# Kernel optimization log

Hardware: AMD Instinct MI355X
Metric: run time of the kernel (lower is better)

The kernel has to match this reference:

```python
import jax, jax.numpy as jnp
import numpy as np

N_NODES = 50000
N_EDGES = 800000
NFEAT, NHID1, NHID2, NHID3, NCLASS = 128, 128, 128, 64, 32


def _glorot(key, fan_in, fan_out):
    lim = 1.0 / np.sqrt(fan_in)
    return jax.random.uniform(key, (fan_in, fan_out), jnp.float32, -lim, lim)


def setup_inputs() -> dict:
    key = jax.random.key(0)
    ks = jax.random.split(key, 12)
    x = jax.random.normal(ks[0], (N_NODES, NFEAT), jnp.float32)
    edge_src = jax.random.randint(ks[1], (N_EDGES,), 0, N_NODES, jnp.int32)
    edge_dst = jax.random.randint(ks[2], (N_EDGES,), 0, N_NODES, jnp.int32)
    edge_val = jax.random.uniform(ks[3], (N_EDGES,), jnp.float32)
    W1 = _glorot(ks[4], NFEAT, NHID1)
    W2 = _glorot(ks[5], NHID1, NHID2)
    W3 = _glorot(ks[6], NHID2, NHID3)
    W4 = _glorot(ks[7], NHID3, NCLASS)
    b1 = jnp.zeros((NHID1,), jnp.float32)
    b2 = jnp.zeros((NHID2,), jnp.float32)
    b3 = jnp.zeros((NHID3,), jnp.float32)
    b4 = jnp.zeros((NCLASS,), jnp.float32)
    return {"x": x, "edge_src": edge_src, "edge_dst": edge_dst, "edge_val": edge_val,
            "W1": W1, "b1": b1, "W2": W2, "b2": b2, "W3": W3, "b3": b3, "W4": W4, "b4": b4}


def _gc_layer(h, W, b, src, dst, val):
    # support = h @ W ; out = adj @ support + b  (adj in COO form)
    support = h @ W                                   # [N, d_out]
    msgs = support[src] * val[:, None]                # [E, d_out] irregular gather
    agg = jax.ops.segment_sum(msgs, dst, num_segments=N_NODES)  # scatter-add
    return agg + b


def reference(x, edge_src, edge_dst, edge_val, W1, b1, W2, b2, W3, b3, W4, b4):
    h = jax.nn.relu(_gc_layer(x, W1, b1, edge_src, edge_dst, edge_val))
    h = jax.nn.relu(_gc_layer(h, W2, b2, edge_src, edge_dst, edge_val))
    h = jax.nn.relu(_gc_layer(h, W3, b3, edge_src, edge_dst, edge_val))
    h = _gc_layer(h, W4, b4, edge_src, edge_dst, edge_val)
    return h
```

## Files before the change

kernel.cpp:

```cpp
#include <hip/hip_runtime.h>

constexpr int NNODES = 50000;
constexpr int NEDGES = 800000;
constexpr int CAP = 64;

constexpr int NPART = 8;
constexpr int PSIZE = NNODES / NPART;
constexpr int FCH = 2048;
constexpr int QCAP = 640;

constexpr int CHUNKS = (NEDGES + FCH - 1) / FCH;
constexpr int TILE_ITEMS = (NNODES + 63) / 64;
constexpr int PACK_TOT = 43008;

typedef __attribute__((ext_vector_type(8))) short short8;
typedef __attribute__((ext_vector_type(8))) unsigned short ushort8;
typedef __attribute__((ext_vector_type(4))) float f32x4;

__device__ __forceinline__ unsigned short f2b(float f) {
    unsigned int u = __float_as_uint(f);
    u += 0x7FFFu + ((u >> 16) & 1u);
    return (unsigned short)(u >> 16);
}
__device__ __forceinline__ float b2f(unsigned short u) {
    return __uint_as_float(((unsigned int)u) << 16);
}
__device__ __forceinline__ float recval(unsigned int rec) {
    return __uint_as_float(rec & 0xFFFF0000u);
}

template <int N, int K>
__device__ __forceinline__ void pack_one(int idx, const float* __restrict__ W,
                                         unsigned short* __restrict__ Wp) {
    constexpr int KS = K / 32;
    int j = idx & 7;
    int lane = (idx >> 3) & 63;
    int t = idx >> 9;
    int nt = t / KS, ks = t % KS;
    int n = nt * 16 + (lane & 15);
    int k = ks * 32 + (lane >> 4) * 8 + j;
    Wp[idx] = f2b(W[(size_t)k * N + n]);
}

__global__ __launch_bounds__(256) void prep_kernel(
        const float* __restrict__ W1, const float* __restrict__ W2,
        const float* __restrict__ W3, const float* __restrict__ W4,
        unsigned short* __restrict__ Wp1, unsigned short* __restrict__ Wp2,
        unsigned short* __restrict__ Wp3, unsigned short* __restrict__ Wp4) {
    int p = blockIdx.x * 256 + threadIdx.x;
    if (p < 16384) pack_one<128, 128>(p, W1, Wp1);
    else if (p < 32768) pack_one<128, 128>(p - 16384, W2, Wp2);
    else if (p < 40960) pack_one<64, 128>(p - 32768, W3, Wp3);
    else if (p < 43008) pack_one<32, 64>(p - 40960, W4, Wp4);
}

template <int N, int K, bool AF32>
__device__ __forceinline__ void gemm_item(int t, const void* __restrict__ Hv,
                                          const unsigned short* __restrict__ Wp,
                                          unsigned short* __restrict__ Sb) {
    constexpr int NT = N / 16, KS = K / 32;
    const int lane = threadIdx.x & 63;
    const int wave = threadIdx.x >> 6;
    const int waveRow = t * 64 + wave * 16;
    const int m = lane & 15, quad = lane >> 4;
    int arow = waveRow + m;
    if (arow >= NNODES) arow = NNODES - 1;

    f32x4 acc[NT];
#pragma unroll
    for (int nt = 0; nt < NT; ++nt) acc[nt] = (f32x4){0.f, 0.f, 0.f, 0.f};

#pragma unroll
    for (int ks = 0; ks < KS; ++ks) {
        short8 a;
        if (AF32) {
            const float* hp = (const float*)Hv + (size_t)arow * K + ks * 32 + quad * 8;
            float4 a0 = *reinterpret_cast<const float4*>(hp);
            float4 a1 = *reinterpret_cast<const float4*>(hp + 4);
            a[0] = (short)f2b(a0.x); a[1] = (short)f2b(a0.y);
            a[2] = (short)f2b(a0.z); a[3] = (short)f2b(a0.w);
            a[4] = (short)f2b(a1.x); a[5] = (short)f2b(a1.y);
            a[6] = (short)f2b(a1.z); a[7] = (short)f2b(a1.w);
        } else {
            a = *reinterpret_cast<const short8*>(
                (const unsigned short*)Hv + (size_t)arow * K + ks * 32 + quad * 8);
        }
#pragma unroll
        for (int nt = 0; nt < NT; ++nt) {
            short8 b = *reinterpret_cast<const short8*>(Wp + ((nt * KS + ks) * 64 + lane) * 8);
            acc[nt] = __builtin_amdgcn_mfma_f32_16x16x32_bf16(a, b, acc[nt], 0, 0, 0);
        }
    }

#pragma unroll
    for (int reg = 0; reg < 4; ++reg) {
        int grow = waveRow + quad * 4 + reg;
        if (grow < NNODES) {
#pragma unroll
            for (int nt = 0; nt < NT; ++nt)
                Sb[(size_t)grow * N + nt * 16 + m] = f2b(acc[nt][reg]);
        }
    }
}

__global__ __launch_bounds__(256) void fill_gemm1_kernel(
        const int* __restrict__ src, const int* __restrict__ dst,
        const float* __restrict__ val, int* __restrict__ cursor,
        unsigned int* __restrict__ buckets,
        const float* __restrict__ x, const unsigned short* __restrict__ Wp1,
        unsigned short* __restrict__ Q) {
    __shared__ unsigned int q_rec[QCAP];
    __shared__ int q_d[QCAP];
    __shared__ int qcount;

    const int g = blockIdx.x / 10;
    const int r = blockIdx.x % 10;
    if (r >= 8) {
        gemm_item<128, 128, true>(g * 2 + (r - 8), x, Wp1, Q);
        return;
    }

    if (threadIdx.x == 0) qcount = 0;
    __syncthreads();

    const int part = blockIdx.x & 7;
    const int lo = part * PSIZE, hi = lo + PSIZE;
    const int e0 = g * FCH + threadIdx.x * 8;

    int dd[8], ss[8];
    float vv[8];
    if (e0 + 7 < NEDGES) {
        int4 d4a = *reinterpret_cast<const int4*>(dst + e0);
        int4 d4b = *reinterpret_cast<const int4*>(dst + e0 + 4);
        int4 s4a = *reinterpret_cast<const int4*>(src + e0);
        int4 s4b = *reinterpret_cast<const int4*>(src + e0 + 4);
        float4 v4a = *reinterpret_cast<const float4*>(val + e0);
        float4 v4b = *reinterpret_cast<const float4*>(val + e0 + 4);
        dd[0] = d4a.x; dd[1] = d4a.y; dd[2] = d4a.z; dd[3] = d4a.w;
        dd[4] = d4b.x; dd[5] = d4b.y; dd[6] = d4b.z; dd[7] = d4b.w;
        ss[0] = s4a.x; ss[1] = s4a.y; ss[2] = s4a.z; ss[3] = s4a.w;
        ss[4] = s4b.x; ss[5] = s4b.y; ss[6] = s4b.z; ss[7] = s4b.w;
        vv[0] = v4a.x; vv[1] = v4a.y; vv[2] = v4a.z; vv[3] = v4a.w;
        vv[4] = v4b.x; vv[5] = v4b.y; vv[6] = v4b.z; vv[7] = v4b.w;
    } else {
#pragma unroll
        for (int i = 0; i < 8; ++i) {
            int e = e0 + i;
            if (e < NEDGES) { dd[i] = dst[e]; ss[i] = src[e]; vv[i] = val[e]; }
            else { dd[i] = -1; ss[i] = 0; vv[i] = 0.f; }
        }
    }
#pragma unroll
    for (int i = 0; i < 8; ++i) {
        int d = dd[i];
        if (d >= lo && d < hi) {
            unsigned int rec = (unsigned int)ss[i] | ((unsigned int)f2b(vv[i]) << 16);
            int pos = atomicAdd(&qcount, 1);
            if (pos < QCAP) {
                q_rec[pos] = rec;
                q_d[pos] = d;
            } else {
                int p = atomicAdd(&cursor[d], 1);
                if (p < CAP) buckets[(size_t)d * CAP + p] = rec;
            }
        }
    }
    __syncthreads();

    int n = qcount < QCAP ? qcount : QCAP;
    for (int i = threadIdx.x; i < n; i += 256) {
        int d = q_d[i];
        unsigned int rec = q_rec[i];
        int p = atomicAdd(&cursor[d], 1);
        if (p < CAP) buckets[(size_t)d * CAP + p] = rec;
    }
}

template <int NIN, int NOUT>
__global__ __launch_bounds__(256) void agg_gemm_kernel(
        const unsigned short* __restrict__ Sprev, const unsigned int* __restrict__ buckets,
        const int* __restrict__ counts, const float* __restrict__ bias,
        const unsigned short* __restrict__ Wp, unsigned short* __restrict__ Snext) {
    constexpr int NCH = NIN / 8;
    constexpr int R = 256 / NCH;
    constexpr int LROW = NIN + 8;
    constexpr int KS = NIN / 32;
    constexpr int NT = NOUT / 16;
    constexpr int RT = R / 16;
    constexpr int TILES = RT * NT;
    __shared__ unsigned short htile[R * LROW];

    const int nodeBase = blockIdx.x * R;

    {
        int nl = threadIdx.x / NCH;
        int cg = threadIdx.x % NCH;
        int node = nodeBase + nl;
        float acc[8];
        if (node < NNODES) {
#pragma unroll
            for (int t = 0; t < 8; ++t) acc[t] = bias[cg * 8 + t];
            int cnt = counts[node];
            if (cnt > CAP) cnt = CAP;
            const unsigned int* eb = buckets + (size_t)node * CAP;
            int j = 0;
            for (; j + 8 <= cnt; j += 8) {
                uint4 ea = *reinterpret_cast<const uint4*>(eb + j);
                uint4 ec = *reinterpret_cast<const uint4*>(eb + j + 4);
                const ushort8 m0 = *reinterpret_cast<const ushort8*>(Sprev + (size_t)(ea.x & 0xFFFF) * NIN + cg * 8);
                const ushort8 m1 = *reinterpret_cast<const ushort8*>(Sprev + (size_t)(ea.y & 0xFFFF) * NIN + cg * 8);
                const ushort8 m2 = *reinterpret_cast<const ushort8*>(Sprev + (size_t)(ea.z & 0xFFFF) * NIN + cg * 8);
                const ushort8 m3 = *reinterpret_cast<const ushort8*>(Sprev + (size_t)(ea.w & 0xFFFF) * NIN + cg * 8);
                const ushort8 m4 = *reinterpret_cast<const ushort8*>(Sprev + (size_t)(ec.x & 0xFFFF) * NIN + cg * 8);
                const ushort8 m5 = *reinterpret_cast<const ushort8*>(Sprev + (size_t)(ec.y & 0xFFFF) * NIN + cg * 8);
                const ushort8 m6 = *reinterpret_cast<const ushort8*>(Sprev + (size_t)(ec.z & 0xFFFF) * NIN + cg * 8);
                const ushort8 m7 = *reinterpret_cast<const ushort8*>(Sprev + (size_t)(ec.w & 0xFFFF) * NIN + cg * 8);
#pragma unroll
                for (int t = 0; t < 8; ++t) {
                    acc[t] = fmaf(b2f(m0[t]), recval(ea.x), acc[t]);
                    acc[t] = fmaf(b2f(m1[t]), recval(ea.y), acc[t]);
                    acc[t] = fmaf(b2f(m2[t]), recval(ea.z), acc[t]);
                    acc[t] = fmaf(b2f(m3[t]), recval(ea.w), acc[t]);
                    acc[t] = fmaf(b2f(m4[t]), recval(ec.x), acc[t]);
                    acc[t] = fmaf(b2f(m5[t]), recval(ec.y), acc[t]);
                    acc[t] = fmaf(b2f(m6[t]), recval(ec.z), acc[t]);
                    acc[t] = fmaf(b2f(m7[t]), recval(ec.w), acc[t]);
                }
            }
            for (; j + 4 <= cnt; j += 4) {
                uint4 ea = *reinterpret_cast<const uint4*>(eb + j);
                const ushort8 m0 = *reinterpret_cast<const ushort8*>(Sprev + (size_t)(ea.x & 0xFFFF) * NIN + cg * 8);
                const ushort8 m1 = *reinterpret_cast<const ushort8*>(Sprev + (size_t)(ea.y & 0xFFFF) * NIN + cg * 8);
                const ushort8 m2 = *reinterpret_cast<const ushort8*>(Sprev + (size_t)(ea.z & 0xFFFF) * NIN + cg * 8);
                const ushort8 m3 = *reinterpret_cast<const ushort8*>(Sprev + (size_t)(ea.w & 0xFFFF) * NIN + cg * 8);
#pragma unroll
                for (int t = 0; t < 8; ++t) {
                    acc[t] = fmaf(b2f(m0[t]), recval(ea.x), acc[t]);
                    acc[t] = fmaf(b2f(m1[t]), recval(ea.y), acc[t]);
                    acc[t] = fmaf(b2f(m2[t]), recval(ea.z), acc[t]);
                    acc[t] = fmaf(b2f(m3[t]), recval(ea.w), acc[t]);
                }
            }
            for (; j < cnt; ++j) {
                unsigned int rec = eb[j];
                float v = recval(rec);
                const ushort8 mr = *reinterpret_cast<const ushort8*>(Sprev + (size_t)(rec & 0xFFFF) * NIN + cg * 8);
#pragma unroll
                for (int t = 0; t < 8; ++t) acc[t] = fmaf(b2f(mr[t]), v, acc[t]);
            }
        } else {
#pragma unroll
            for (int t = 0; t < 8; ++t) acc[t] = 0.f;
        }
        ushort8 o;
#pragma unroll
        for (int t = 0; t < 8; ++t) o[t] = f2b(fmaxf(acc[t], 0.f));
        *reinterpret_cast<ushort8*>(&htile[nl * LROW + cg * 8]) = o;
    }
    __syncthreads();

    {
        const int lane = threadIdx.x & 63, wave = threadIdx.x >> 6;
        const int m = lane & 15, quad = lane >> 4;
        for (int t = wave; t < TILES; t += 4) {
            int rt = t / NT, nt = t % NT;
            f32x4 acc = (f32x4){0.f, 0.f, 0.f, 0.f};
#pragma unroll
            for (int ks = 0; ks < KS; ++ks) {
                short8 a = *reinterpret_cast<const short8*>(
                    &htile[(rt * 16 + m) * LROW + ks * 32 + quad * 8]);
                short8 b = *reinterpret_cast<const short8*>(Wp + ((nt * KS + ks) * 64 + lane) * 8);
                acc = __builtin_amdgcn_mfma_f32_16x16x32_bf16(a, b, acc, 0, 0, 0);
            }
#pragma unroll
            for (int reg = 0; reg < 4; ++reg) {
                int grow = nodeBase + rt * 16 + quad * 4 + reg;
                if (grow < NNODES)
                    Snext[(size_t)grow * NOUT + nt * 16 + m] = f2b(acc[reg]);
            }
        }
    }
}

__global__ __launch_bounds__(256) void agg_out_kernel(const unsigned short* __restrict__ Sb,
        const unsigned int* __restrict__ buckets, const int* __restrict__ counts,
        const float* __restrict__ bias, float* __restrict__ outp) {
    constexpr int N = 32;
    int node = blockIdx.x * 64 + threadIdx.x / 4;
    int cg = threadIdx.x % 4;
    if (node >= NNODES) return;
    int cnt = counts[node];
    if (cnt > CAP) cnt = CAP;
    const unsigned int* eb = buckets + (size_t)node * CAP;
    float acc[8];
#pragma unroll
    for (int t = 0; t < 8; ++t) acc[t] = bias[cg * 8 + t];

    int j = 0;
    for (; j + 8 <= cnt; j += 8) {
        uint4 ea = *reinterpret_cast<const uint4*>(eb + j);
        uint4 ec = *reinterpret_cast<const uint4*>(eb + j + 4);
        const ushort8 m0 = *reinterpret_cast<const ushort8*>(Sb + (size_t)(ea.x & 0xFFFF) * N + cg * 8);
        const ushort8 m1 = *reinterpret_cast<const ushort8*>(Sb + (size_t)(ea.y & 0xFFFF) * N + cg * 8);
        const ushort8 m2 = *reinterpret_cast<const ushort8*>(Sb + (size_t)(ea.z & 0xFFFF) * N + cg * 8);
        const ushort8 m3 = *reinterpret_cast<const ushort8*>(Sb + (size_t)(ea.w & 0xFFFF) * N + cg * 8);
        const ushort8 m4 = *reinterpret_cast<const ushort8*>(Sb + (size_t)(ec.x & 0xFFFF) * N + cg * 8);
        const ushort8 m5 = *reinterpret_cast<const ushort8*>(Sb + (size_t)(ec.y & 0xFFFF) * N + cg * 8);
        const ushort8 m6 = *reinterpret_cast<const ushort8*>(Sb + (size_t)(ec.z & 0xFFFF) * N + cg * 8);
        const ushort8 m7 = *reinterpret_cast<const ushort8*>(Sb + (size_t)(ec.w & 0xFFFF) * N + cg * 8);
#pragma unroll
        for (int t = 0; t < 8; ++t) {
            acc[t] = fmaf(b2f(m0[t]), recval(ea.x), acc[t]);
            acc[t] = fmaf(b2f(m1[t]), recval(ea.y), acc[t]);
            acc[t] = fmaf(b2f(m2[t]), recval(ea.z), acc[t]);
            acc[t] = fmaf(b2f(m3[t]), recval(ea.w), acc[t]);
            acc[t] = fmaf(b2f(m4[t]), recval(ec.x), acc[t]);
            acc[t] = fmaf(b2f(m5[t]), recval(ec.y), acc[t]);
            acc[t] = fmaf(b2f(m6[t]), recval(ec.z), acc[t]);
            acc[t] = fmaf(b2f(m7[t]), recval(ec.w), acc[t]);
        }
    }
    for (; j + 4 <= cnt; j += 4) {
        uint4 ea = *reinterpret_cast<const uint4*>(eb + j);
        const ushort8 m0 = *reinterpret_cast<const ushort8*>(Sb + (size_t)(ea.x & 0xFFFF) * N + cg * 8);
        const ushort8 m1 = *reinterpret_cast<const ushort8*>(Sb + (size_t)(ea.y & 0xFFFF) * N + cg * 8);
        const ushort8 m2 = *reinterpret_cast<const ushort8*>(Sb + (size_t)(ea.z & 0xFFFF) * N + cg * 8);
        const ushort8 m3 = *reinterpret_cast<const ushort8*>(Sb + (size_t)(ea.w & 0xFFFF) * N + cg * 8);
#pragma unroll
        for (int t = 0; t < 8; ++t) {
            acc[t] = fmaf(b2f(m0[t]), recval(ea.x), acc[t]);
            acc[t] = fmaf(b2f(m1[t]), recval(ea.y), acc[t]);
            acc[t] = fmaf(b2f(m2[t]), recval(ea.z), acc[t]);
            acc[t] = fmaf(b2f(m3[t]), recval(ea.w), acc[t]);
        }
    }
    for (; j < cnt; ++j) {
        unsigned int rec = eb[j];
        float v = recval(rec);
        const ushort8 mr = *reinterpret_cast<const ushort8*>(Sb + (size_t)(rec & 0xFFFF) * N + cg * 8);
#pragma unroll
        for (int t = 0; t < 8; ++t) acc[t] = fmaf(b2f(mr[t]), v, acc[t]);
    }

    float* op = outp + (size_t)node * N + cg * 8;
    *reinterpret_cast<float4*>(op) = make_float4(acc[0], acc[1], acc[2], acc[3]);
    *reinterpret_cast<float4*>(op + 4) = make_float4(acc[4], acc[5], acc[6], acc[7]);
}

extern "C" void kernel_launch(void* const* d_in, const int* in_sizes, int n_in,
                              void* d_out, int out_size, void* d_ws, size_t ws_size,
                              hipStream_t stream) {
    const float* x   = (const float*)d_in[0];
    const int*   src = (const int*)d_in[1];
    const int*   dst = (const int*)d_in[2];
    const float* val = (const float*)d_in[3];
    const float* W1  = (const float*)d_in[4];
    const float* b1  = (const float*)d_in[5];
    const float* W2  = (const float*)d_in[6];
    const float* b2  = (const float*)d_in[7];
    const float* W3  = (const float*)d_in[8];
    const float* b3  = (const float*)d_in[9];
    const float* W4  = (const float*)d_in[10];
    const float* b4  = (const float*)d_in[11];
    float* out = (float*)d_out;

    unsigned short* P = (unsigned short*)d_ws;
    unsigned short* Q = P + (size_t)NNODES * 128;
    unsigned int* buckets = (unsigned int*)(Q + (size_t)NNODES * 128);
    unsigned short* Wp1 = (unsigned short*)(buckets + (size_t)NNODES * CAP);
    unsigned short* Wp2 = Wp1 + 128 * 128;
    unsigned short* Wp3 = Wp2 + 128 * 128;
    unsigned short* Wp4 = Wp3 + 128 * 64;
    int* cursor = (int*)(Wp4 + 64 * 32);

    const dim3 blk(256);

    hipMemsetAsync(cursor, 0, NNODES * sizeof(int), stream);
    prep_kernel<<<(PACK_TOT + 255) / 256, blk, 0, stream>>>(W1, W2, W3, W4,
                                                            Wp1, Wp2, Wp3, Wp4);
    fill_gemm1_kernel<<<CHUNKS * 10, blk, 0, stream>>>(
        src, dst, val, cursor, buckets, x, Wp1, Q);
    agg_gemm_kernel<128, 128><<<(NNODES + 15) / 16, blk, 0, stream>>>(
        Q, buckets, cursor, b1, Wp2, P);
    agg_gemm_kernel<128, 64><<<(NNODES + 15) / 16, blk, 0, stream>>>(
        P, buckets, cursor, b2, Wp3, Q);
    agg_gemm_kernel<64, 32><<<(NNODES + 31) / 32, blk, 0, stream>>>(
        Q, buckets, cursor, b3, Wp4, P);
    agg_out_kernel<<<(NNODES + 63) / 64, blk, 0, stream>>>(P, buckets, cursor, b4, out);
}
```

Measured before the change: 221.4 us.

## Fold weight packing into fill kernel and stage W1 in LDS per GEMM block

Result: slower. 239.6 us (+8.2%).

```diff
diff --git a/kernel.cpp b/kernel.cpp
--- a/kernel.cpp
+++ b/kernel.cpp
@@ -10,12 +10,14 @@
 constexpr int QCAP = 640;
 
 constexpr int CHUNKS = (NEDGES + FCH - 1) / FCH;
-constexpr int TILE_ITEMS = (NNODES + 63) / 64;
-constexpr int PACK_TOT = 43008;
+constexpr int PACK234 = 26624;
+constexpr int PACK_BLOCKS = (PACK234 + 255) / 256;
 
 typedef __attribute__((ext_vector_type(8))) short short8;
 typedef __attribute__((ext_vector_type(8))) unsigned short ushort8;
 typedef __attribute__((ext_vector_type(4))) float f32x4;
+typedef __attribute__((ext_vector_type(4))) int i32x4;
+typedef __attribute__((ext_vector_type(4))) unsigned int u32x4;
 
 __device__ __forceinline__ unsigned short f2b(float f) {
     unsigned int u = __float_as_uint(f);
@@ -42,22 +44,10 @@
     Wp[idx] = f2b(W[(size_t)k * N + n]);
 }
 
-__global__ __launch_bounds__(256) void prep_kernel(
-        const float* __restrict__ W1, const float* __restrict__ W2,
-        const float* __restrict__ W3, const float* __restrict__ W4,
-        unsigned short* __restrict__ Wp1, unsigned short* __restrict__ Wp2,
-        unsigned short* __restrict__ Wp3, unsigned short* __restrict__ Wp4) {
-    int p = blockIdx.x * 256 + threadIdx.x;
-    if (p < 16384) pack_one<128, 128>(p, W1, Wp1);
-    else if (p < 32768) pack_one<128, 128>(p - 16384, W2, Wp2);
-    else if (p < 40960) pack_one<64, 128>(p - 32768, W3, Wp3);
-    else if (p < 43008) pack_one<32, 64>(p - 40960, W4, Wp4);
-}
-
-template <int N, int K, bool AF32>
-__device__ __forceinline__ void gemm_item(int t, const void* __restrict__ Hv,
-                                          const unsigned short* __restrict__ Wp,
-                                          unsigned short* __restrict__ Sb) {
+template <int N, int K>
+__device__ __forceinline__ void gemm_item_lds(int t, const float* __restrict__ H,
+                                              const unsigned short* __restrict__ wlds,
+                                              unsigned short* __restrict__ Sb) {
     constexpr int NT = N / 16, KS = K / 32;
     const int lane = threadIdx.x & 63;
     const int wave = threadIdx.x >> 6;
@@ -72,22 +62,17 @@
 
 #pragma unroll
     for (int ks = 0; ks < KS; ++ks) {
+        const float* hp = H + (size_t)arow * K + ks * 32 + quad * 8;
+        f32x4 a0 = __builtin_nontemporal_load(reinterpret_cast<const f32x4*>(hp));
+        f32x4 a1 = __builtin_nontemporal_load(reinterpret_cast<const f32x4*>(hp + 4));
         short8 a;
-        if (AF32) {
-            const float* hp = (const float*)Hv + (size_t)arow * K + ks * 32 + quad * 8;
-            float4 a0 = *reinterpret_cast<const float4*>(hp);
-            float4 a1 = *reinterpret_cast<const float4*>(hp + 4);
-            a[0] = (short)f2b(a0.x); a[1] = (short)f2b(a0.y);
-            a[2] = (short)f2b(a0.z); a[3] = (short)f2b(a0.w);
-            a[4] = (short)f2b(a1.x); a[5] = (short)f2b(a1.y);
-            a[6] = (short)f2b(a1.z); a[7] = (short)f2b(a1.w);
-        } else {
-            a = *reinterpret_cast<const short8*>(
-                (const unsigned short*)Hv + (size_t)arow * K + ks * 32 + quad * 8);
-        }
+        a[0] = (short)f2b(a0.x); a[1] = (short)f2b(a0.y);
+        a[2] = (short)f2b(a0.z); a[3] = (short)f2b(a0.w);
+        a[4] = (short)f2b(a1.x); a[5] = (short)f2b(a1.y);
+        a[6] = (short)f2b(a1.z); a[7] = (short)f2b(a1.w);
 #pragma unroll
         for (int nt = 0; nt < NT; ++nt) {
-            short8 b = *reinterpret_cast<const short8*>(Wp + ((nt * KS + ks) * 64 + lane) * 8);
+            short8 b = *reinterpret_cast<const short8*>(wlds + ((nt * KS + ks) * 64 + lane) * 8);
             acc[nt] = __builtin_amdgcn_mfma_f32_16x16x32_bf16(a, b, acc[nt], 0, 0, 0);
         }
     }
@@ -107,19 +92,45 @@
         const int* __restrict__ src, const int* __restrict__ dst,
         const float* __restrict__ val, int* __restrict__ cursor,
         unsigned int* __restrict__ buckets,
-        const float* __restrict__ x, const unsigned short* __restrict__ Wp1,
-        unsigned short* __restrict__ Q) {
-    __shared__ unsigned int q_rec[QCAP];
-    __shared__ int q_d[QCAP];
+        const float* __restrict__ x, const float* __restrict__ W1,
+        unsigned short* __restrict__ Q,
+        const float* __restrict__ W2, const float* __restrict__ W3,
+        const float* __restrict__ W4,
+        unsigned short* __restrict__ Wp2, unsigned short* __restrict__ Wp3,
+        unsigned short* __restrict__ Wp4) {
+    __shared__ __align__(16) unsigned int smem[8192];
     __shared__ int qcount;
+
+    const int total10 = CHUNKS * 10;
+    if (blockIdx.x >= total10) {
+        int p = (blockIdx.x - total10) * 256 + threadIdx.x;
+        if (p < 16384) pack_one<128, 128>(p, W2, Wp2);
+        else if (p < 24576) pack_one<64, 128>(p - 16384, W3, Wp3);
+        else if (p < 26624) pack_one<32, 64>(p - 24576, W4, Wp4);
+        return;
+    }
 
     const int g = blockIdx.x / 10;
     const int r = blockIdx.x % 10;
+
     if (r >= 8) {
-        gemm_item<128, 128, true>(g * 2 + (r - 8), x, Wp1, Q);
+        unsigned short* wlds = (unsigned short*)smem;
+        for (int idx = threadIdx.x; idx < 16384; idx += 256) {
+            int j = idx & 7;
+            int lane = (idx >> 3) & 63;
+            int t = idx >> 9;
+            int nt = t / 4, ks = t % 4;
+            int n = nt * 16 + (lane & 15);
+            int k = ks * 32 + (lane >> 4) * 8 + j;
+            wlds[idx] = f2b(W1[(size_t)k * 128 + n]);
+        }
+        __syncthreads();
+        gemm_item_lds<128, 128>(g * 2 + (r - 8), x, wlds, Q);
         return;
     }
 
+    unsigned int* q_rec = smem;
+    int* q_d = (int*)smem + QCAP;
     if (threadIdx.x == 0) qcount = 0;
     __syncthreads();
 
@@ -130,12 +141,12 @@
     int dd[8], ss[8];
     float vv[8];
     if (e0 + 7 < NEDGES) {
-        int4 d4a = *reinterpret_cast<const int4*>(dst + e0);
-        int4 d4b = *reinterpret_cast<const int4*>(dst + e0 + 4);
-        int4 s4a = *reinterpret_cast<const int4*>(src + e0);
-        int4 s4b = *reinterpret_cast<const int4*>(src + e0 + 4);
-        float4 v4a = *reinterpret_cast<const float4*>(val + e0);
-        float4 v4b = *reinterpret_cast<const float4*>(val + e0 + 4);
+        i32x4 d4a = __builtin_nontemporal_load(reinterpret_cast<const i32x4*>(dst + e0));
+        i32x4 d4b = __builtin_nontemporal_load(reinterpret_cast<const i32x4*>(dst + e0 + 4));
+        i32x4 s4a = __builtin_nontemporal_load(reinterpret_cast<const i32x4*>(src + e0));
+        i32x4 s4b = __builtin_nontemporal_load(reinterpret_cast<const i32x4*>(src + e0 + 4));
+        f32x4 v4a = __builtin_nontemporal_load(reinterpret_cast<const f32x4*>(val + e0));
+        f32x4 v4b = __builtin_nontemporal_load(reinterpret_cast<const f32x4*>(val + e0 + 4));
         dd[0] = d4a.x; dd[1] = d4a.y; dd[2] = d4a.z; dd[3] = d4a.w;
         dd[4] = d4b.x; dd[5] = d4b.y; dd[6] = d4b.z; dd[7] = d4b.w;
         ss[0] = s4a.x; ss[1] = s4a.y; ss[2] = s4a.z; ss[3] = s4a.w;
@@ -367,19 +378,16 @@
     unsigned short* P = (unsigned short*)d_ws;
     unsigned short* Q = P + (size_t)NNODES * 128;
     unsigned int* buckets = (unsigned int*)(Q + (size_t)NNODES * 128);
-    unsigned short* Wp1 = (unsigned short*)(buckets + (size_t)NNODES * CAP);
-    unsigned short* Wp2 = Wp1 + 128 * 128;
+    unsigned short* Wp2 = (unsigned short*)(buckets + (size_t)NNODES * CAP);
     unsigned short* Wp3 = Wp2 + 128 * 128;
     unsigned short* Wp4 = Wp3 + 128 * 64;
     int* cursor = (int*)(Wp4 + 64 * 32);
 
     const dim3 blk(256);
 
-    hipMemsetAsync(cursor, 0, NNODES * sizeof(int), stream);
-    prep_kernel<<<(PACK_TOT + 255) / 256, blk, 0, stream>>>(W1, W2, W3, W4,
-                                                            Wp1, Wp2, Wp3, Wp4);
-    fill_gemm1_kernel<<<CHUNKS * 10, blk, 0, stream>>>(
-        src, dst, val, cursor, buckets, x, Wp1, Q);
+    (void)hipMemsetAsync(cursor, 0, NNODES * sizeof(int), stream);
+    fill_gemm1_kernel<<<CHUNKS * 10 + PACK_BLOCKS, blk, 0, stream>>>(
+        src, dst, val, cursor, buckets, x, W1, Q, W2, W3, W4, Wp2, Wp3, Wp4);
     agg_gemm_kernel<128, 128><<<(NNODES + 15) / 16, blk, 0, stream>>>(
         Q, buckets, cursor, b1, Wp2, P);
     agg_gemm_kernel<128, 64><<<(NNODES + 15) / 16, blk, 0, stream>>>(
```
